# Performance work log

Measured on AMD Instinct MI355X. Metric: run time of the kernel, lower is better.

Reference implementation:

```python
import jax, jax.numpy as jnp
import numpy as np

N = 50000      # nodes
E = 800000     # edges (avg degree 16)
IN = 128       # in_features
OUT = 64       # out_features
NEG_SLOPE = 0.2


def setup_inputs() -> dict:
    key = jax.random.key(0)
    ks = jax.random.split(key, 6)
    x = jax.random.normal(ks[0], (N, IN), dtype=jnp.float32)
    edge_src = jax.random.randint(ks[1], (E,), 0, N, dtype=jnp.int32)  # row i of adj
    edge_dst = jax.random.randint(ks[2], (E,), 0, N, dtype=jnp.int32)  # col j of adj
    stdv = 1.0 / np.sqrt(OUT)
    W = jax.random.uniform(ks[3], (IN, OUT), jnp.float32, -stdv, stdv)
    a = jax.random.uniform(ks[4], (2 * OUT, 1), jnp.float32, -stdv, stdv)
    bias = jax.random.uniform(ks[5], (OUT,), jnp.float32, -stdv, stdv)
    return {"x": x, "W": W, "a": a, "bias": bias,
            "edge_src": edge_src, "edge_dst": edge_dst}


def reference(x, W, a, bias, edge_src, edge_dst):
    # h = input @ weight + bias    [N, OUT]
    h = x @ W + bias
    # Per-node attention halves: Wh1[i] + Wh2[j] == (e = Wh1 + Wh2.T)[i, j]
    Wh1 = h @ a[:OUT, 0]   # [N]
    Wh2 = h @ a[OUT:, 0]   # [N]
    # Edge-centric scores only where adj is nonzero (mirrors e.sparse_mask(adj))
    e = jax.nn.leaky_relu(Wh1[edge_src] + Wh2[edge_dst], NEG_SLOPE)  # [E]
    # Sparse softmax over dim=1 -> segment softmax grouped by source row
    emax = jax.ops.segment_max(e, edge_src, num_segments=N)          # [N]
    ex = jnp.exp(e - emax[edge_src])                                 # [E]
    denom = jax.ops.segment_sum(ex, edge_src, num_segments=N)        # [N]
    alpha = ex / denom[edge_src]                                     # [E]
    # out[i] = sum_j alpha_ij * h[j]  (sparse attention @ h)
    out = jax.ops.segment_sum(alpha[:, None] * h[edge_dst], edge_src,
                              num_segments=N)                        # [N, OUT]
    return out
```

## Files before the change

kernel.cpp:

```cpp
#include <hip/hip_runtime.h>
#include <math.h>


typedef unsigned long long u64;
typedef unsigned int u32;

namespace {
constexpr int NN   = 50000;
constexpr int EE   = 800000;
constexpr int INF_ = 128;
constexpr int OUTF = 64;
constexpr float NEG_SLOPE = 0.2f;
constexpr int MAXDEG = 64;

constexpr int NBUCK   = 196;
constexpr int BCAP    = 4608;
constexpr int S1_CHUNK  = 2048;
constexpr int S1_BLOCKS = (EE + S1_CHUNK - 1) / S1_CHUNK;
constexpr int GEMM_BLOCKS = (NN + 127) / 128;
constexpr int K1_BLOCKS = S1_BLOCKS + GEMM_BLOCKS;
constexpr int AGG_BLOCKS = (NN + 63) / 64;
}

static __device__ __forceinline__ u32 pack2bf(float a, float b) {
    u32 xa = __builtin_bit_cast(u32, a), xb = __builtin_bit_cast(u32, b);
    xa = (xa + 0x7fffu + ((xa >> 16) & 1u)) >> 16;
    xb = (xb + 0x7fffu + ((xb >> 16) & 1u)) >> 16;
    return xa | (xb << 16);
}

__global__ __launch_bounds__(256)
void gat_fused(const float* __restrict__ x, const float* __restrict__ W,
               const float* __restrict__ av, const float* __restrict__ bias,
               const int* __restrict__ esrc, const int* __restrict__ edst,
               u32* __restrict__ h16, float* __restrict__ wh1,
               float* __restrict__ wh2, int* __restrict__ bcnt_g,
               u64* __restrict__ bdata)
{
    __shared__ u64 smem[3072];
    const int id  = blockIdx.x;
    const int tid = threadIdx.x;
    const int ridx = id >> 1;
    const bool is_gemm = (id & 1) == 0;

    if (!is_gemm) {
        u64* s_pairs = smem;
        int* s_bcnt  = (int*)((char*)smem + 16384);
        int* s_scan  = s_bcnt + NBUCK;
        int* s_goff  = s_scan + NBUCK;

        for (int i = tid; i < NBUCK; i += 256) s_bcnt[i] = 0;
        __syncthreads();

        const int e0  = ridx * S1_CHUNK;
        const int tot = (EE - e0) < S1_CHUNK ? (EE - e0) : S1_CHUNK;

        int mb[8], mp[8]; u64 mv[8]; int nmine = 0;
#pragma unroll
        for (int k = 0; k < 8; ++k) {
            const int e = e0 + tid + k * 256;
            if (e < e0 + tot) {
                const int s = esrc[e], d = edst[e];
                const int b = s >> 8;
                mb[nmine] = b;
                mp[nmine] = atomicAdd(&s_bcnt[b], 1);
                mv[nmine] = ((u64)(u32)d << 32) | (u32)s;
                ++nmine;
            }
        }
        __syncthreads();
        if (tid < NBUCK) s_scan[tid] = s_bcnt[tid];
        __syncthreads();
        for (int off = 1; off < NBUCK; off <<= 1) {
            int v = 0;
            if (tid < NBUCK && tid >= off) v = s_scan[tid - off];
            __syncthreads();
            if (tid < NBUCK && tid >= off) s_scan[tid] += v;
            __syncthreads();
        }
        if (tid < NBUCK) {
            const int c = s_bcnt[tid];
            s_goff[tid] = c > 0 ? atomicAdd(&bcnt_g[tid], c) : 0;
        }
        __syncthreads();
        for (int k = 0; k < nmine; ++k) {
            const int b = mb[k];
            s_pairs[s_scan[b] - s_bcnt[b] + mp[k]] = mv[k];
        }
        __syncthreads();
        for (int i = tid; i < tot; i += 256) {
            const u64 p = s_pairs[i];
            const int s = (int)(u32)(p & 0xffffffffull);
            const int b = s >> 8;
            const int g = s_goff[b] + (i - (s_scan[b] - s_bcnt[b]));
            if (g < BCAP) bdata[(size_t)b * BCAP + g] = p;
        }
        return;
    }

    float* xT = (float*)smem;
    float* Wc = (float*)((char*)smem + 16384);
    const int lane  = tid & 63;
    const int w     = tid >> 6;
    const int node0 = ridx * 128;
    const int ng    = lane & 7;
    const int fg    = lane >> 3;
    const int nbase = w * 32 + ng * 4;
    const int f0    = fg * 8;

    const int srow = tid & 127;
    const int sq   = tid >> 7;
    const int grow = node0 + srow;

    float acc[4][8] = {};

    for (int kc = 0; kc < INF_; kc += 32) {
        __syncthreads();
        {
            float4 v[4];
#pragma unroll
            for (int j = 0; j < 4; ++j) v[j] = make_float4(0.f, 0.f, 0.f, 0.f);
            if (grow < NN) {
                const float4* xr = (const float4*)(x + (size_t)grow * INF_ + kc + sq * 16);
#pragma unroll
                for (int j = 0; j < 4; ++j) v[j] = xr[j];
            }
            float* dst = &xT[(sq * 16) * 128 + srow];
#pragma unroll
            for (int j = 0; j < 4; ++j) {
                dst[(j*4+0)*128] = v[j].x;
                dst[(j*4+1)*128] = v[j].y;
                dst[(j*4+2)*128] = v[j].z;
                dst[(j*4+3)*128] = v[j].w;
            }
        }
        {
            const float4* wr = (const float4*)(W + (size_t)kc * OUTF);
            float4* wc = (float4*)Wc;
            wc[tid]       = wr[tid];
            wc[tid + 256] = wr[tid + 256];
        }
        __syncthreads();
#pragma unroll 4
        for (int kk = 0; kk < 32; ++kk) {
            const float4 xv = *(const float4*)&xT[kk * 128 + nbase];
            const float4 w0 = *(const float4*)&Wc[kk * 64 + f0];
            const float4 w1 = *(const float4*)&Wc[kk * 64 + f0 + 4];
            const float xa[4] = {xv.x, xv.y, xv.z, xv.w};
            const float wa[8] = {w0.x,w0.y,w0.z,w0.w,w1.x,w1.y,w1.z,w1.w};
#pragma unroll
            for (int i = 0; i < 4; ++i)
#pragma unroll
                for (int j = 0; j < 8; ++j) acc[i][j] += xa[i] * wa[j];
        }
    }

    const float4 b0 = ((const float4*)bias)[fg*2];
    const float4 b1 = ((const float4*)bias)[fg*2+1];
    const float4 q0 = ((const float4*)av)[fg*2];
    const float4 q1 = ((const float4*)av)[fg*2+1];
    const float4 r0 = ((const float4*)(av + OUTF))[fg*2];
    const float4 r1 = ((const float4*)(av + OUTF))[fg*2+1];
    const float bb[8]  = {b0.x,b0.y,b0.z,b0.w,b1.x,b1.y,b1.z,b1.w};
    const float a1v[8] = {q0.x,q0.y,q0.z,q0.w,q1.x,q1.y,q1.z,q1.w};
    const float a2v[8] = {r0.x,r0.y,r0.z,r0.w,r1.x,r1.y,r1.z,r1.w};

#pragma unroll
    for (int i = 0; i < 4; ++i) {
        const int node = node0 + nbase + i;
        float p1 = 0.f, p2 = 0.f;
#pragma unroll
        for (int j = 0; j < 8; ++j) {
            acc[i][j] += bb[j];
            p1 += acc[i][j] * a1v[j];
            p2 += acc[i][j] * a2v[j];
        }
        p1 += __shfl_xor(p1, 8); p1 += __shfl_xor(p1, 16); p1 += __shfl_xor(p1, 32);
        p2 += __shfl_xor(p2, 8); p2 += __shfl_xor(p2, 16); p2 += __shfl_xor(p2, 32);
        if (node < NN) {
            const u32 pk0 = pack2bf(acc[i][0], acc[i][1]);
            const u32 pk1 = pack2bf(acc[i][2], acc[i][3]);
            const u32 pk2 = pack2bf(acc[i][4], acc[i][5]);
            const u32 pk3 = pack2bf(acc[i][6], acc[i][7]);
            *(uint4*)&h16[(size_t)node * 32 + fg * 4] = make_uint4(pk0, pk1, pk2, pk3);
            if (fg == 0) { wh1[node] = p1; wh2[node] = p2; }
        }
    }
}

__global__ __launch_bounds__(256)
void gat_agg(const int* __restrict__ bcnt_g, const u64* __restrict__ bdata,
             const float* __restrict__ wh1, const float* __restrict__ wh2,
             const u32* __restrict__ h16, float* __restrict__ out)
{
    __shared__ int   l_dst[64 * 64];
    __shared__ float l_alpha[64 * 64];
    __shared__ int   l_cnt[64];
    const int tid    = threadIdx.x;
    const int bid    = blockIdx.x;
    const int node0  = bid << 6;
    const int bucket = bid >> 2;

    if (tid < 64) l_cnt[tid] = 0;
    __syncthreads();

    int n = bcnt_g[bucket];
    n = n > BCAP ? BCAP : n;
    for (int i = tid; i < n; i += 256) {
        const u64 p = bdata[(size_t)bucket * BCAP + i];
        const int s  = (int)(u32)(p & 0xffffffffull);
        const int ln = s - node0;
        if (ln >= 0 && ln < 64) {
            const int pos = atomicAdd(&l_cnt[ln], 1);
            if (pos < MAXDEG) l_dst[(ln << 6) + pos] = (int)(u32)(p >> 32);
        }
    }
    __syncthreads();

    const int lane = tid & 63;
    const int qw   = (tid >> 6) * 4 + (lane >> 4);
    const int f    = lane & 15;

#pragma unroll
    for (int nl = 0; nl < 4; ++nl) {
        const int li   = qw + 16 * nl;
        const int node = node0 + li;
        int deg = l_cnt[li];
        deg = deg > MAXDEG ? MAXDEG : deg;
        const float w1 = (node < NN) ? wh1[node] : 0.f;

        float el[4]; int dl[4];
        float m = -INFINITY;
#pragma unroll
        for (int k = 0; k < 4; ++k) {
            const int slot = f + 16 * k;
            int d = l_dst[(li << 6) + slot];
            d = (slot < deg) ? d : 0;
            dl[k] = d;
            float v = w1 + wh2[d];
            v = v > 0.f ? v : NEG_SLOPE * v;
            el[k] = (slot < deg) ? v : -INFINITY;
            m = fmaxf(m, el[k]);
        }
        m = fmaxf(m, __shfl_xor(m, 1)); m = fmaxf(m, __shfl_xor(m, 2));
        m = fmaxf(m, __shfl_xor(m, 4)); m = fmaxf(m, __shfl_xor(m, 8));
        float ex[4], s = 0.f;
#pragma unroll
        for (int k = 0; k < 4; ++k) {
            ex[k] = (f + 16 * k < deg) ? __expf(el[k] - m) : 0.f;
            s += ex[k];
        }
        s += __shfl_xor(s, 1); s += __shfl_xor(s, 2);
        s += __shfl_xor(s, 4); s += __shfl_xor(s, 8);
        const float inv = (deg > 0) ? 1.f / s : 0.f;
#pragma unroll
        for (int k = 0; k < 4; ++k) {
            l_alpha[(li << 6) + f + 16 * k] = ex[k] * inv;
            l_dst  [(li << 6) + f + 16 * k] = dl[k];
        }
    }
    __syncthreads();

#pragma unroll
    for (int nl = 0; nl < 4; ++nl) {
        const int li   = qw + 16 * nl;
        const int node = node0 + li;
        int deg = l_cnt[li];
        deg = deg > MAXDEG ? MAXDEG : deg;
        const int base = li << 6;
        float4 acc = make_float4(0.f, 0.f, 0.f, 0.f);
        for (int j0 = 0; j0 < deg; j0 += 4) {
            const float a0 = l_alpha[base + j0];
            const float a1 = l_alpha[base + j0 + 1];
            const float a2 = l_alpha[base + j0 + 2];
            const float a3 = l_alpha[base + j0 + 3];
            const int d0 = l_dst[base + j0],     d1 = l_dst[base + j0 + 1];
            const int d2 = l_dst[base + j0 + 2], d3 = l_dst[base + j0 + 3];
            const uint2 v0 = *(const uint2*)&h16[(size_t)d0 * 32 + f * 2];
            const uint2 v1 = *(const uint2*)&h16[(size_t)d1 * 32 + f * 2];
            const uint2 v2 = *(const uint2*)&h16[(size_t)d2 * 32 + f * 2];
            const uint2 v3 = *(const uint2*)&h16[(size_t)d3 * 32 + f * 2];
#define BF_LO(u) __builtin_bit_cast(float, (u) << 16)
#define BF_HI(u) __builtin_bit_cast(float, (u) & 0xffff0000u)
            acc.x += a0*BF_LO(v0.x) + a1*BF_LO(v1.x) + a2*BF_LO(v2.x) + a3*BF_LO(v3.x);
            acc.y += a0*BF_HI(v0.x) + a1*BF_HI(v1.x) + a2*BF_HI(v2.x) + a3*BF_HI(v3.x);
            acc.z += a0*BF_LO(v0.y) + a1*BF_LO(v1.y) + a2*BF_LO(v2.y) + a3*BF_LO(v3.y);
            acc.w += a0*BF_HI(v0.y) + a1*BF_HI(v1.y) + a2*BF_HI(v2.y) + a3*BF_HI(v3.y);
#undef BF_LO
#undef BF_HI
        }
        if (node < NN)
            *(float4*)&out[(size_t)node * OUTF + f * 4] = acc;
    }
}

extern "C" void kernel_launch(void* const* d_in, const int* in_sizes, int n_in,
                              void* d_out, int out_size, void* d_ws, size_t ws_size,
                              hipStream_t stream)
{
    const float* x    = (const float*)d_in[0];
    const float* W    = (const float*)d_in[1];
    const float* av   = (const float*)d_in[2];
    const float* bias = (const float*)d_in[3];
    const int*   esrc = (const int*)d_in[4];
    const int*   edst = (const int*)d_in[5];
    float* out = (float*)d_out;

    u32*   h16    = (u32*)d_ws;
    float* wh1    = (float*)(h16 + (size_t)NN * 32);
    float* wh2    = wh1 + NN;
    int*   bcnt_g = (int*)(wh2 + NN);
    u64*   bdata  = (u64*)(bcnt_g + 200);

    hipMemsetAsync(bcnt_g, 0, NBUCK * sizeof(int), stream);
    gat_fused<<<K1_BLOCKS, 256, 0, stream>>>(
        x, W, av, bias, esrc, edst, h16, wh1, wh2, bcnt_g, bdata);
    gat_agg<<<AGG_BLOCKS, 256, 0, stream>>>(bcnt_g, bdata, wh1, wh2, h16, out);
}
```

Baseline: 135.0 us.

## Use split-bf16 MFMA for the GEMM, pad bucket counters, deepen gather unroll

The FP32 FMA GEMM in the fused kernel is replaced by MFMA 16x16x32 bf16 instructions. Each operand is split into hi and lo bf16 parts and three products are summed to keep near-FP32 accuracy. W is pre-swizzled into LDS in both halves, and the epilogue is rewritten around the MFMA output layout. Bucket counters are padded to 16-int stride to reduce atomic contention from false sharing, and the aggregation gather loop is unrolled to 8 loads in flight. The risks are extra conversion ALU work, a larger shared-memory footprint, and reading past deg when it is not a multiple of 8, since those padded slots are read regardless.

```diff
diff --git a/kernel.cpp b/kernel.cpp
--- a/kernel.cpp
+++ b/kernel.cpp
@@ -4,6 +4,9 @@
 
 typedef unsigned long long u64;
 typedef unsigned int u32;
+typedef unsigned short u16;
+typedef __attribute__((ext_vector_type(8))) short bf16x8;
+typedef __attribute__((ext_vector_type(4))) float f32x4;
 
 namespace {
 constexpr int NN   = 50000;
@@ -14,6 +17,7 @@
 constexpr int MAXDEG = 64;
 
 constexpr int NBUCK   = 196;
+constexpr int BSTRIDE = 16;
 constexpr int BCAP    = 4608;
 constexpr int S1_CHUNK  = 2048;
 constexpr int S1_BLOCKS = (EE + S1_CHUNK - 1) / S1_CHUNK;
@@ -22,11 +26,15 @@
 constexpr int AGG_BLOCKS = (NN + 63) / 64;
 }
 
+static __device__ __forceinline__ u16 bf16rne(float v) {
+    u32 u = __builtin_bit_cast(u32, v);
+    return (u16)((u + 0x7fffu + ((u >> 16) & 1u)) >> 16);
+}
+static __device__ __forceinline__ float bf2f(u16 b) {
+    return __builtin_bit_cast(float, (u32)b << 16);
+}
 static __device__ __forceinline__ u32 pack2bf(float a, float b) {
-    u32 xa = __builtin_bit_cast(u32, a), xb = __builtin_bit_cast(u32, b);
-    xa = (xa + 0x7fffu + ((xa >> 16) & 1u)) >> 16;
-    xb = (xb + 0x7fffu + ((xb >> 16) & 1u)) >> 16;
-    return xa | (xb << 16);
+    return (u32)bf16rne(a) | ((u32)bf16rne(b) << 16);
 }
 
 __global__ __launch_bounds__(256)
@@ -37,7 +45,7 @@
                float* __restrict__ wh2, int* __restrict__ bcnt_g,
                u64* __restrict__ bdata)
 {
-    __shared__ u64 smem[3072];
+    __shared__ u64 smem[4096];
     const int id  = blockIdx.x;
     const int tid = threadIdx.x;
     const int ridx = id >> 1;
@@ -80,7 +88,7 @@
         }
         if (tid < NBUCK) {
             const int c = s_bcnt[tid];
-            s_goff[tid] = c > 0 ? atomicAdd(&bcnt_g[tid], c) : 0;
+            s_goff[tid] = c > 0 ? atomicAdd(&bcnt_g[tid * BSTRIDE], c) : 0;
         }
         __syncthreads();
         for (int k = 0; k < nmine; ++k) {
@@ -98,92 +106,120 @@
         return;
     }
 
-    float* xT = (float*)smem;
-    float* Wc = (float*)((char*)smem + 16384);
-    const int lane  = tid & 63;
-    const int w     = tid >> 6;
-    const int node0 = ridx * 128;
-    const int ng    = lane & 7;
-    const int fg    = lane >> 3;
-    const int nbase = w * 32 + ng * 4;
-    const int f0    = fg * 8;
-
-    const int srow = tid & 127;
-    const int sq   = tid >> 7;
-    const int grow = node0 + srow;
-
-    float acc[4][8] = {};
-
-    for (int kc = 0; kc < INF_; kc += 32) {
-        __syncthreads();
-        {
-            float4 v[4];
-#pragma unroll
-            for (int j = 0; j < 4; ++j) v[j] = make_float4(0.f, 0.f, 0.f, 0.f);
-            if (grow < NN) {
-                const float4* xr = (const float4*)(x + (size_t)grow * INF_ + kc + sq * 16);
-#pragma unroll
-                for (int j = 0; j < 4; ++j) v[j] = xr[j];
-            }
-            float* dst = &xT[(sq * 16) * 128 + srow];
-#pragma unroll
-            for (int j = 0; j < 4; ++j) {
-                dst[(j*4+0)*128] = v[j].x;
-                dst[(j*4+1)*128] = v[j].y;
-                dst[(j*4+2)*128] = v[j].z;
-                dst[(j*4+3)*128] = v[j].w;
-            }
-        }
-        {
-            const float4* wr = (const float4*)(W + (size_t)kc * OUTF);
-            float4* wc = (float4*)Wc;
-            wc[tid]       = wr[tid];
-            wc[tid + 256] = wr[tid + 256];
-        }
-        __syncthreads();
-#pragma unroll 4
-        for (int kk = 0; kk < 32; ++kk) {
-            const float4 xv = *(const float4*)&xT[kk * 128 + nbase];
-            const float4 w0 = *(const float4*)&Wc[kk * 64 + f0];
-            const float4 w1 = *(const float4*)&Wc[kk * 64 + f0 + 4];
-            const float xa[4] = {xv.x, xv.y, xv.z, xv.w};
-            const float wa[8] = {w0.x,w0.y,w0.z,w0.w,w1.x,w1.y,w1.z,w1.w};
-#pragma unroll
-            for (int i = 0; i < 4; ++i)
-#pragma unroll
-                for (int j = 0; j < 8; ++j) acc[i][j] += xa[i] * wa[j];
-        }
-    }
-
-    const float4 b0 = ((const float4*)bias)[fg*2];
-    const float4 b1 = ((const float4*)bias)[fg*2+1];
-    const float4 q0 = ((const float4*)av)[fg*2];
-    const float4 q1 = ((const float4*)av)[fg*2+1];
-    const float4 r0 = ((const float4*)(av + OUTF))[fg*2];
-    const float4 r1 = ((const float4*)(av + OUTF))[fg*2+1];
-    const float bb[8]  = {b0.x,b0.y,b0.z,b0.w,b1.x,b1.y,b1.z,b1.w};
-    const float a1v[8] = {q0.x,q0.y,q0.z,q0.w,q1.x,q1.y,q1.z,q1.w};
-    const float a2v[8] = {r0.x,r0.y,r0.z,r0.w,r1.x,r1.y,r1.z,r1.w};
+    u32* Whi = (u32*)smem;
+    u32* Wlo = Whi + 4096;
 
 #pragma unroll
     for (int i = 0; i < 4; ++i) {
-        const int node = node0 + nbase + i;
-        float p1 = 0.f, p2 = 0.f;
-#pragma unroll
-        for (int j = 0; j < 8; ++j) {
-            acc[i][j] += bb[j];
-            p1 += acc[i][j] * a1v[j];
-            p2 += acc[i][j] * a2v[j];
-        }
-        p1 += __shfl_xor(p1, 8); p1 += __shfl_xor(p1, 16); p1 += __shfl_xor(p1, 32);
-        p2 += __shfl_xor(p2, 8); p2 += __shfl_xor(p2, 16); p2 += __shfl_xor(p2, 32);
-        if (node < NN) {
-            const u32 pk0 = pack2bf(acc[i][0], acc[i][1]);
-            const u32 pk1 = pack2bf(acc[i][2], acc[i][3]);
-            const u32 pk2 = pack2bf(acc[i][4], acc[i][5]);
-            const u32 pk3 = pack2bf(acc[i][6], acc[i][7]);
-            *(uint4*)&h16[(size_t)node * 32 + fg * 4] = make_uint4(pk0, pk1, pk2, pk3);
-            if (fg == 0) { wh1[node] = p1; wh2[node] = p2; }
+        const int idx    = tid * 4 + i;
+        const int lane_s = idx & 63;
+        const int kt_s   = (idx >> 6) & 3;
+        const int nt_s   = idx >> 8;
+        const int n  = nt_s * 16 + (lane_s & 15);
+        const int k0 = kt_s * 32 + (lane_s >> 4) * 8;
+        u32 hw[4], lw[4];
+#pragma unroll
+        for (int jp = 0; jp < 4; ++jp) {
+            const float va = W[(k0 + 2*jp    ) * OUTF + n];
+            const float vb = W[(k0 + 2*jp + 1) * OUTF + n];
+            const u16 hA = bf16rne(va); const u16 lA = bf16rne(va - bf2f(hA));
+            const u16 hB = bf16rne(vb); const u16 lB = bf16rne(vb - bf2f(hB));
+            hw[jp] = (u32)hA | ((u32)hB << 16);
+            lw[jp] = (u32)lA | ((u32)lB << 16);
+        }
+        const int off = ((nt_s * 4 + kt_s) * 64 + lane_s) * 4;
+        *(uint4*)&Whi[off] = make_uint4(hw[0], hw[1], hw[2], hw[3]);
+        *(uint4*)&Wlo[off] = make_uint4(lw[0], lw[1], lw[2], lw[3]);
+    }
+    __syncthreads();
+
+    const int lane = tid & 63;
+    const int w    = tid >> 6;
+    const int n15  = lane & 15;
+    const int quad = lane >> 4;
+    const int node0  = ridx * 128;
+    const int nodeA0 = node0 + w * 32;
+
+    f32x4 acc[2][4];
+#pragma unroll
+    for (int mt = 0; mt < 2; ++mt)
+#pragma unroll
+        for (int nt = 0; nt < 4; ++nt) acc[mt][nt] = (f32x4)(0.f);
+
+    for (int kt = 0; kt < 4; ++kt) {
+        bf16x8 Ahi[2], Alo[2];
+#pragma unroll
+        for (int mt = 0; mt < 2; ++mt) {
+            const int node = nodeA0 + mt * 16 + n15;
+            float v[8] = {0.f,0.f,0.f,0.f,0.f,0.f,0.f,0.f};
+            if (node < NN) {
+                const float4* xr = (const float4*)(x + (size_t)node * INF_ + kt * 32 + quad * 8);
+                const float4 p = xr[0], q = xr[1];
+                v[0]=p.x; v[1]=p.y; v[2]=p.z; v[3]=p.w;
+                v[4]=q.x; v[5]=q.y; v[6]=q.z; v[7]=q.w;
+            }
+#pragma unroll
+            for (int j = 0; j < 8; ++j) {
+                const u16 hb = bf16rne(v[j]);
+                const u16 lb = bf16rne(v[j] - bf2f(hb));
+                Ahi[mt][j] = (short)hb;
+                Alo[mt][j] = (short)lb;
+            }
+        }
+#pragma unroll
+        for (int nt = 0; nt < 4; ++nt) {
+            const int off = ((nt * 4 + kt) * 64 + lane) * 4;
+            const bf16x8 Bhi = *(const bf16x8*)&Whi[off];
+            const bf16x8 Blo = *(const bf16x8*)&Wlo[off];
+#pragma unroll
+            for (int mt = 0; mt < 2; ++mt) {
+                acc[mt][nt] = __builtin_amdgcn_mfma_f32_16x16x32_bf16(Ahi[mt], Bhi, acc[mt][nt], 0, 0, 0);
+                acc[mt][nt] = __builtin_amdgcn_mfma_f32_16x16x32_bf16(Ahi[mt], Blo, acc[mt][nt], 0, 0, 0);
+                acc[mt][nt] = __builtin_amdgcn_mfma_f32_16x16x32_bf16(Alo[mt], Bhi, acc[mt][nt], 0, 0, 0);
+            }
+        }
+    }
+
+#pragma unroll
+    for (int mt = 0; mt < 2; ++mt) {
+        float p1[4] = {0.f,0.f,0.f,0.f}, p2[4] = {0.f,0.f,0.f,0.f};
+        float hv[4][4];
+#pragma unroll
+        for (int nt = 0; nt < 4; ++nt) {
+            const int feat = nt * 16 + n15;
+            const float bv = bias[feat];
+            const float A1 = av[feat];
+            const float A2 = av[OUTF + feat];
+#pragma unroll
+            for (int r = 0; r < 4; ++r) {
+                const float d = acc[mt][nt][r] + bv;
+                hv[nt][r] = d;
+                p1[r] += d * A1;
+                p2[r] += d * A2;
+            }
+        }
+#pragma unroll
+        for (int r = 0; r < 4; ++r) {
+            p1[r] += __shfl_xor(p1[r], 1); p1[r] += __shfl_xor(p1[r], 2);
+            p1[r] += __shfl_xor(p1[r], 4); p1[r] += __shfl_xor(p1[r], 8);
+            p2[r] += __shfl_xor(p2[r], 1); p2[r] += __shfl_xor(p2[r], 2);
+            p2[r] += __shfl_xor(p2[r], 4); p2[r] += __shfl_xor(p2[r], 8);
+        }
+#pragma unroll
+        for (int r = 0; r < 4; ++r) {
+            float pk[4];
+#pragma unroll
+            for (int nt = 0; nt < 4; ++nt) pk[nt] = __shfl_xor(hv[nt][r], 1);
+            const int node = nodeA0 + mt * 16 + quad * 4 + r;
+            if (node < NN) {
+                if ((n15 & 1) == 0) {
+#pragma unroll
+                    for (int nt = 0; nt < 4; ++nt)
+                        h16[(size_t)node * 32 + nt * 8 + (n15 >> 1)] =
+                            pack2bf(hv[nt][r], pk[nt]);
+                }
+                if (n15 == 0) { wh1[node] = p1[r]; wh2[node] = p2[r]; }
+            }
         }
     }
 }
@@ -204,7 +240,7 @@
     if (tid < 64) l_cnt[tid] = 0;
     __syncthreads();
 
-    int n = bcnt_g[bucket];
+    int n = bcnt_g[bucket * BSTRIDE];
     n = n > BCAP ? BCAP : n;
     for (int i = tid; i < n; i += 256) {
         const u64 p = bdata[(size_t)bucket * BCAP + i];
@@ -269,23 +305,25 @@
         deg = deg > MAXDEG ? MAXDEG : deg;
         const int base = li << 6;
         float4 acc = make_float4(0.f, 0.f, 0.f, 0.f);
-        for (int j0 = 0; j0 < deg; j0 += 4) {
-            const float a0 = l_alpha[base + j0];
-            const float a1 = l_alpha[base + j0 + 1];
-            const float a2 = l_alpha[base + j0 + 2];
-            const float a3 = l_alpha[base + j0 + 3];
-            const int d0 = l_dst[base + j0],     d1 = l_dst[base + j0 + 1];
-            const int d2 = l_dst[base + j0 + 2], d3 = l_dst[base + j0 + 3];
-            const uint2 v0 = *(const uint2*)&h16[(size_t)d0 * 32 + f * 2];
-            const uint2 v1 = *(const uint2*)&h16[(size_t)d1 * 32 + f * 2];
-            const uint2 v2 = *(const uint2*)&h16[(size_t)d2 * 32 + f * 2];
-            const uint2 v3 = *(const uint2*)&h16[(size_t)d3 * 32 + f * 2];
+        for (int j0 = 0; j0 < deg; j0 += 8) {
+            float aa[8]; int dd[8]; uint2 vv[8];
+#pragma unroll
+            for (int k = 0; k < 8; ++k) {
+                aa[k] = l_alpha[base + j0 + k];
+                dd[k] = l_dst[base + j0 + k];
+            }
+#pragma unroll
+            for (int k = 0; k < 8; ++k)
+                vv[k] = *(const uint2*)&h16[(size_t)dd[k] * 32 + f * 2];
 #define BF_LO(u) __builtin_bit_cast(float, (u) << 16)
 #define BF_HI(u) __builtin_bit_cast(float, (u) & 0xffff0000u)
-            acc.x += a0*BF_LO(v0.x) + a1*BF_LO(v1.x) + a2*BF_LO(v2.x) + a3*BF_LO(v3.x);
-            acc.y += a0*BF_HI(v0.x) + a1*BF_HI(v1.x) + a2*BF_HI(v2.x) + a3*BF_HI(v3.x);
-            acc.z += a0*BF_LO(v0.y) + a1*BF_LO(v1.y) + a2*BF_LO(v2.y) + a3*BF_LO(v3.y);
-            acc.w += a0*BF_HI(v0.y) + a1*BF_HI(v1.y) + a2*BF_HI(v2.y) + a3*BF_HI(v3.y);
+#pragma unroll
+            for (int k = 0; k < 8; ++k) {
+                acc.x += aa[k] * BF_LO(vv[k].x);
+                acc.y += aa[k] * BF_HI(vv[k].x);
+                acc.z += aa[k] * BF_LO(vv[k].y);
+                acc.w += aa[k] * BF_HI(vv[k].y);
+            }
 #undef BF_LO
 #undef BF_HI
         }
@@ -310,9 +348,9 @@
     float* wh1    = (float*)(h16 + (size_t)NN * 32);
     float* wh2    = wh1 + NN;
     int*   bcnt_g = (int*)(wh2 + NN);
-    u64*   bdata  = (u64*)(bcnt_g + 200);
-
-    hipMemsetAsync(bcnt_g, 0, NBUCK * sizeof(int), stream);
+    u64*   bdata  = (u64*)(bcnt_g + NBUCK * BSTRIDE + 64);
+
+    hipMemsetAsync(bcnt_g, 0, NBUCK * BSTRIDE * sizeof(int), stream);
     gat_fused<<<K1_BLOCKS, 256, 0, stream>>>(
         x, W, av, bias, esrc, edst, h16, wh1, wh2, bcnt_g, bdata);
     gat_agg<<<AGG_BLOCKS, 256, 0, stream>>>(bcnt_g, bdata, wh1, wh2, h16, out);
```

Result: faster. 121.9 us (-9.7%).
